# Optimization experiments

Hardware: AMD Instinct MI355X
Metric: run time of the kernel (lower is better)

Reference implementation:

```python
import jax, jax.numpy as jnp
import numpy as np

K = 4
N_UP = 50
N_DOWN = 50


def setup_inputs() -> dict:
    key = jax.random.key(0)
    k1, k2, k3, k4 = jax.random.split(key, 4)
    B, N, D = 2048, 100, 128
    configs = jax.random.randint(k1, (B, N), 0, 4, dtype=jnp.int64)
    tok_table = jax.random.normal(k2, (4, D), dtype=jnp.float32)
    pos_table = jax.random.normal(k3, (144, D), dtype=jnp.float32)
    W_orb = jax.random.normal(k4, (K * (N_UP + N_DOWN), D), dtype=jnp.float32) * 0.01
    b_orb = jnp.zeros((K * (N_UP + N_DOWN),), dtype=jnp.float32)
    return {"configs": configs, "tok_table": tok_table, "pos_table": pos_table,
            "W_orb": W_orb, "b_orb": b_orb}


def _occ_idx(mask, n_occ):
    # indices of occupied sites first (stable argsort of -mask), then sorted ascending
    idx = jnp.argsort(-mask.astype(jnp.float32), axis=1)[:, :n_occ]
    return jnp.sort(idx, axis=1)


def reference(configs, tok_table, pos_table, W_orb, b_orb):
    B, N = configs.shape
    # encode_input + identity backbone
    h = tok_table[configs] + pos_table[jnp.arange(N)][None, :, :]  # (B,N,D)
    orb = jnp.einsum('bnd,od->bno', h, W_orb) + b_orb               # (B,N,K*(nu+nd))
    orb_up = orb[..., :K * N_UP].reshape(B, N, K, N_UP).transpose(0, 2, 1, 3)
    orb_dn = orb[..., K * N_UP:].reshape(B, N, K, N_DOWN).transpose(0, 2, 1, 3)
    has_up = (configs == 1) | (configs == 3)
    has_dn = (configs == 2) | (configs == 3)
    up_idx = _occ_idx(has_up, N_UP)      # (B,n_up)
    dn_idx = _occ_idx(has_dn, N_DOWN)    # (B,n_down)
    phi_up = jnp.take_along_axis(orb_up, up_idx[:, None, :, None], axis=2)  # (B,K,nu,nu)
    phi_dn = jnp.take_along_axis(orb_dn, dn_idx[:, None, :, None], axis=2)  # (B,K,nd,nd)
    det_up = jnp.linalg.det(phi_up)  # (B,K)
    det_dn = jnp.linalg.det(phi_dn)  # (B,K)
    psi = jnp.sum(det_up * det_dn, axis=1)  # (B,)
    log_abs = jnp.log(jnp.abs(psi) + 1e-30)
    phase = jnp.where(psi >= 0, 0.0, jnp.pi).astype(jnp.float32)
    return jax.lax.complex(log_abs.astype(jnp.float32), phase)
```

## Files before the change

kernel.cpp:

```cpp
#include <hip/hip_runtime.h>
#include <math.h>

#define NSITE 100
#define NOCC  50
#define DIM   128
#define KDET  4
#define NTAB  400
#define TP_FLOATS ((4 + 144) * NTAB)


__device__ __forceinline__ unsigned dpp_max64_to_lane63(unsigned x) {
  unsigned t;
  t = (unsigned)__builtin_amdgcn_update_dpp((int)x, (int)x, 0x111, 0xf, 0xf, false);
  x = x > t ? x : t;
  t = (unsigned)__builtin_amdgcn_update_dpp((int)x, (int)x, 0x112, 0xf, 0xf, false);
  x = x > t ? x : t;
  t = (unsigned)__builtin_amdgcn_update_dpp((int)x, (int)x, 0x114, 0xf, 0xf, false);
  x = x > t ? x : t;
  t = (unsigned)__builtin_amdgcn_update_dpp((int)x, (int)x, 0x118, 0xf, 0xf, false);
  x = x > t ? x : t;
  t = (unsigned)__builtin_amdgcn_update_dpp((int)x, (int)x, 0x142, 0xa, 0xf, false);
  x = x > t ? x : t;
  t = (unsigned)__builtin_amdgcn_update_dpp((int)x, (int)x, 0x143, 0xc, 0xf, false);
  x = x > t ? x : t;
  return x;
}

#define REPB(X) X(0) X(1) X(2) X(3) X(4) X(5) X(6) X(7) X(8) X(9) \
  X(10) X(11) X(12) X(13) X(14) X(15) X(16) X(17) X(18) X(19) \
  X(20) X(21) X(22) X(23) X(24) X(25) X(26) X(27) X(28) X(29) \
  X(30) X(31) X(32) X(33) X(34) X(35) X(36) X(37) X(38) X(39) \
  X(40) X(41) X(42) X(43) X(44) X(45) X(46) X(47) X(48) X(49)

#define LUPAIR(X) \
  X(0,1) X(1,2) X(2,3) X(3,4) X(4,5) X(5,6) X(6,7) X(7,8) X(8,9) X(9,10) \
  X(10,11) X(11,12) X(12,13) X(13,14) X(14,15) X(15,16) X(16,17) X(17,18) \
  X(18,19) X(19,20) X(20,21) X(21,22) X(22,23) X(23,24) X(24,25) X(25,26) \
  X(26,27) X(27,28) X(28,29) X(29,30) X(30,31) X(31,32) X(32,33) X(33,34) \
  X(34,35) X(35,36) X(36,37) X(37,38) X(38,39) X(39,40) X(40,41) X(41,42) \
  X(42,43) X(43,44) X(44,45) X(45,46) X(46,47) X(47,48) X(48,49)

__global__ __launch_bounds__(256) void tp_kernel(
    const float* __restrict__ tok, const float* __restrict__ pos,
    const float* __restrict__ W,   const float* __restrict__ bvec,
    float* __restrict__ T, float* __restrict__ P)
{
  const int gid = blockIdx.x * 256 + threadIdx.x;
  if (gid >= 148 * NTAB) return;
  const int row = gid / NTAB;
  const int col = gid - row * NTAB;
  const float4* h4 = (const float4*)((row < 4) ? (tok + (size_t)row * DIM)
                                               : (pos + (size_t)(row - 4) * DIM));
  const float4* w4 = (const float4*)(W + (size_t)col * DIM);
  float acc = 0.0f;
  #pragma unroll
  for (int i = 0; i < DIM / 4; ++i) {
    float4 a = h4[i], b = w4[i];
    acc = fmaf(a.x, b.x, acc);
    acc = fmaf(a.y, b.y, acc);
    acc = fmaf(a.z, b.z, acc);
    acc = fmaf(a.w, b.w, acc);
  }
  if (row < 4) T[(size_t)row * NTAB + col] = acc;
  else         P[(size_t)(row - 4) * NTAB + col] = acc + bvec[col];
}

__global__ __launch_bounds__(256)
__attribute__((amdgpu_waves_per_eu(7)))
void det_kernel(
    const int*   __restrict__ configs,
    const float* __restrict__ T,
    const float* __restrict__ P,
    double*      __restrict__ dets)
{
  const int b    = blockIdx.x;
  const int spin = blockIdx.y;

  __shared__ int cfg[NSITE];
  __shared__ int idx[NOCC];
  __shared__ unsigned long long omask[2];

  const int tid = threadIdx.x;

  bool occv = false;
  if (tid < NSITE) {
    const int c = configs[(size_t)b * NSITE + tid];
    cfg[tid] = c;
    occv = (spin == 0) ? (c == 1 || c == 3) : (c == 2 || c == 3);
  }
  const unsigned long long bal = __ballot(occv);
  if ((tid & 63) == 0 && tid < 128) omask[tid >> 6] = bal;
  __syncthreads();
  if (tid < NSITE) {
    const unsigned long long m0 = omask[0], m1 = omask[1];
    const int mtot = __popcll(m0) + __popcll(m1);
    const int need = (mtot < NOCC) ? (NOCC - mtot) : 0;
    int pocc;
    if (tid >= 64) pocc = __popcll(m0) + __popcll(m1 & ((1ull << (tid - 64)) - 1ull));
    else           pocc = __popcll(m0 & ((1ull << tid) - 1ull));
    const int punocc = tid - pocc;
    const bool sel = occv ? (pocc < NOCC) : (punocc < need);
    const int  poscap = (pocc  < NOCC) ? pocc  : NOCC;
    const int  pfill  = (punocc < need) ? punocc : need;
    if (sel) idx[poscap + pfill] = tid;
  }
  __syncthreads();

  const int lane = tid & 63;
  const int wave = tid >> 6;
  const int wave_u  = __builtin_amdgcn_readfirstlane(wave);
  const int colbase = spin * 200 + wave_u * 50;

  const bool act  = (lane < NOCC);
  const int  site = idx[act ? lane : 0];
  const int  cc0  = cfg[site];
  const float2* T2 = (const float2*)(T + (size_t)cc0  * NTAB + colbase);
  const float2* P2 = (const float2*)(P + (size_t)site * NTAB + colbase);

  #define DECLQ(i) float q##i;
  REPB(DECLQ)
  #undef DECLQ
  #define LQ(i0, i1) { float2 a = T2[(i0) / 2], c = P2[(i0) / 2]; \
      q##i0 = a.x + c.x; q##i1 = a.y + c.y; }
  LQ(0, 1)  LQ(2, 3)  LQ(4, 5)  LQ(6, 7)  LQ(8, 9)  LQ(10, 11)
  __builtin_amdgcn_sched_barrier(0);
  LQ(12, 13) LQ(14, 15) LQ(16, 17) LQ(18, 19) LQ(20, 21) LQ(22, 23)
  __builtin_amdgcn_sched_barrier(0);
  LQ(24, 25) LQ(26, 27) LQ(28, 29) LQ(30, 31) LQ(32, 33) LQ(34, 35)
  __builtin_amdgcn_sched_barrier(0);
  LQ(36, 37) LQ(38, 39) LQ(40, 41) LQ(42, 43) LQ(44, 45) LQ(46, 47)
  __builtin_amdgcn_sched_barrier(0);
  LQ(48, 49)
  #undef LQ

  #define ZEROQ(i) q##i = act ? q##i : 0.0f;
  REPB(ZEROQ)
  #undef ZEROQ

  unsigned aliveq = act ? 0xFFFFFFFFu : 0u;
  float    mant_prod = 1.0f;
  int      esum = 0;
  unsigned sgnx = 0u;
  unsigned long long chosen = 0ull;
  int      invsum = 0;
  const unsigned lu = (unsigned)lane;

  unsigned keyv;
  int   p;
  float rp;

  #define PIVFIN(Jx) { \
    p = __builtin_amdgcn_readlane((int)keyv, 63) & 63; \
    const float piv = __int_as_float( \
        __builtin_amdgcn_readlane(__float_as_int(q##Jx), p)); \
    const unsigned pb = __float_as_uint(piv); \
    esum += (int)((pb >> 23) & 0xFFu) - 127; \
    sgnx ^= (pb & 0x80000000u); \
    mant_prod *= __uint_as_float((pb & 0x007FFFFFu) | 0x3F800000u); \
    invsum += __popcll(chosen >> (p + 1)); \
    chosen |= 1ull << (unsigned)p; \
    aliveq = ((unsigned)lane == (unsigned)p) ? 0u : aliveq; \
    float r0 = __builtin_amdgcn_rcpf(piv); \
    r0 = fmaf(fmaf(-piv, r0, 1.0f), r0, r0); \
    rp = ((pb & 0x7FFFFFFFu) != 0u) ? r0 : 0.0f; }

  #define UPDC(CC) if ((CC) > cJ1) { \
      const float pc = __int_as_float( \
          __builtin_amdgcn_readlane(__float_as_int(q##CC), p)); \
      q##CC = fmaf(-mult, pc, q##CC); }

  #define LUS(J, J1) { \
    const float mult = __uint_as_float(__float_as_uint(q##J * rp) & aliveq); \
    { const float pc0 = __int_as_float( \
          __builtin_amdgcn_readlane(__float_as_int(q##J1), p)); \
      q##J1 = fmaf(-mult, pc0, q##J1); } \
    keyv = ((__float_as_uint(q##J1) & 0x7FFFFFC0u) | lu) & aliveq; \
    keyv = dpp_max64_to_lane63(keyv); \
    const int cJ1 = (J1); \
    REPB(UPDC) \
    PIVFIN(J1) \
  }

  keyv = ((__float_as_uint(q0) & 0x7FFFFFC0u) | lu) & aliveq;
  keyv = dpp_max64_to_lane63(keyv);
  PIVFIN(0)
  LUPAIR(LUS)
  #undef LUS
  #undef UPDC
  #undef PIVFIN

  const double logdet =
      log((double)mant_prod) + (double)esum * 0.6931471805599453;
  const int sgn = (((sgnx >> 31) + (unsigned)invsum) & 1u) ? -1 : 1;

  if (lane == 0) {
    size_t o = (((size_t)b * 2 + spin) * KDET + wave) * 2;
    dets[o]     = logdet;
    dets[o + 1] = (double)sgn;
  }
}

__global__ __launch_bounds__(256) void combine_kernel(
    const double* __restrict__ dets, float* __restrict__ out, int B)
{
  int b = blockIdx.x * blockDim.x + threadIdx.x;
  if (b >= B) return;
  const double* du = dets + ((size_t)b * 2 + 0) * KDET * 2;
  const double* dd = dets + ((size_t)b * 2 + 1) * KDET * 2;
  double t[KDET], s[KDET], m = -1e300;
  #pragma unroll
  for (int k = 0; k < KDET; ++k) {
    t[k] = du[2 * k] + dd[2 * k];
    s[k] = du[2 * k + 1] * dd[2 * k + 1];
    if (t[k] > m) m = t[k];
  }
  double sum = 0.0;
  #pragma unroll
  for (int k = 0; k < KDET; ++k) {
    if (t[k] > -1e290) sum += s[k] * exp(t[k] - m);
  }
  double p  = (m > -1e290) ? exp(m) * fabs(sum) : 0.0;
  double la = log(p + 1e-30);
  float phase = (sum >= 0.0) ? 0.0f : 3.14159265358979f;
  out[b]     = (float)la;
  out[B + b] = phase;
}

extern "C" void kernel_launch(void* const* d_in, const int* in_sizes, int n_in,
                              void* d_out, int out_size, void* d_ws, size_t ws_size,
                              hipStream_t stream) {
  const int*   configs = (const int*)  d_in[0];
  const float* tok     = (const float*)d_in[1];
  const float* pos     = (const float*)d_in[2];
  const float* W       = (const float*)d_in[3];
  const float* bv      = (const float*)d_in[4];

  float*  wsf  = (float*)d_ws;
  float*  T    = wsf;
  float*  P    = wsf + 4 * NTAB;
  double* dets = (double*)(wsf + TP_FLOATS);
  const int B = in_sizes[0] / NSITE;

  tp_kernel<<<(148 * NTAB + 255) / 256, 256, 0, stream>>>(tok, pos, W, bv, T, P);
  dim3 grid(B, 2);
  det_kernel<<<grid, 256, 0, stream>>>(configs, T, P, dets);
  combine_kernel<<<(B + 255) / 256, 256, 0, stream>>>(dets, (float*)d_out, B);
}
```

Before: 230.0 us.

## Split each 50x50 LU across two waves with LDS-broadcast pivot multipliers

Each determinant's 50 columns are now split across two waves by column parity, so each wave holds 25 registers instead of 50. The grid doubles along z so each block handles two determinants. At every elimination step the owning wave picks the pivot and writes multipliers and pivot metadata to shared memory, and both waves then update their columns. The aim is lower register pressure (waves_per_eu raised to 8) and more parallel waves, at the cost of 50 block-wide barriers per LU and LDS traffic on the serial critical path.

```diff
diff --git a/kernel.cpp b/kernel.cpp
--- a/kernel.cpp
+++ b/kernel.cpp
@@ -26,19 +26,9 @@
   return x;
 }
 
-#define REPB(X) X(0) X(1) X(2) X(3) X(4) X(5) X(6) X(7) X(8) X(9) \
+#define REPC(X) X(0) X(1) X(2) X(3) X(4) X(5) X(6) X(7) X(8) X(9) \
   X(10) X(11) X(12) X(13) X(14) X(15) X(16) X(17) X(18) X(19) \
-  X(20) X(21) X(22) X(23) X(24) X(25) X(26) X(27) X(28) X(29) \
-  X(30) X(31) X(32) X(33) X(34) X(35) X(36) X(37) X(38) X(39) \
-  X(40) X(41) X(42) X(43) X(44) X(45) X(46) X(47) X(48) X(49)
-
-#define LUPAIR(X) \
-  X(0,1) X(1,2) X(2,3) X(3,4) X(4,5) X(5,6) X(6,7) X(7,8) X(8,9) X(9,10) \
-  X(10,11) X(11,12) X(12,13) X(13,14) X(14,15) X(15,16) X(16,17) X(17,18) \
-  X(18,19) X(19,20) X(20,21) X(21,22) X(22,23) X(23,24) X(24,25) X(25,26) \
-  X(26,27) X(27,28) X(28,29) X(29,30) X(30,31) X(31,32) X(32,33) X(33,34) \
-  X(34,35) X(35,36) X(36,37) X(37,38) X(38,39) X(39,40) X(40,41) X(41,42) \
-  X(42,43) X(43,44) X(44,45) X(45,46) X(46,47) X(47,48) X(48,49)
+  X(20) X(21) X(22) X(23) X(24)
 
 __global__ __launch_bounds__(256) void tp_kernel(
     const float* __restrict__ tok, const float* __restrict__ pos,
@@ -66,7 +56,7 @@
 }
 
 __global__ __launch_bounds__(256)
-__attribute__((amdgpu_waves_per_eu(7)))
+__attribute__((amdgpu_waves_per_eu(8)))
 void det_kernel(
     const int*   __restrict__ configs,
     const float* __restrict__ T,
@@ -79,6 +69,8 @@
   __shared__ int cfg[NSITE];
   __shared__ int idx[NOCC];
   __shared__ unsigned long long omask[2];
+  __shared__ float mbuf[2][2][64];
+  __shared__ int   meta[2][2][2];
 
   const int tid = threadIdx.x;
 
@@ -106,35 +98,28 @@
   }
   __syncthreads();
 
-  const int lane = tid & 63;
-  const int wave = tid >> 6;
-  const int wave_u  = __builtin_amdgcn_readfirstlane(wave);
-  const int colbase = spin * 200 + wave_u * 50;
+  const int lane  = tid & 63;
+  const int wave  = tid >> 6;
+  const int dloc  = __builtin_amdgcn_readfirstlane(wave >> 1);
+  const int h     = __builtin_amdgcn_readfirstlane(wave & 1);
+  const int k     = blockIdx.z * 2 + dloc;
+  const int colbase = spin * 200 + k * 50;
 
   const bool act  = (lane < NOCC);
   const int  site = idx[act ? lane : 0];
   const int  cc0  = cfg[site];
-  const float2* T2 = (const float2*)(T + (size_t)cc0  * NTAB + colbase);
-  const float2* P2 = (const float2*)(P + (size_t)site * NTAB + colbase);
+  const float* Trow = T + (size_t)cc0  * NTAB + colbase + h;
+  const float* Prow = P + (size_t)site * NTAB + colbase + h;
 
   #define DECLQ(i) float q##i;
-  REPB(DECLQ)
+  REPC(DECLQ)
   #undef DECLQ
-  #define LQ(i0, i1) { float2 a = T2[(i0) / 2], c = P2[(i0) / 2]; \
-      q##i0 = a.x + c.x; q##i1 = a.y + c.y; }
-  LQ(0, 1)  LQ(2, 3)  LQ(4, 5)  LQ(6, 7)  LQ(8, 9)  LQ(10, 11)
-  __builtin_amdgcn_sched_barrier(0);
-  LQ(12, 13) LQ(14, 15) LQ(16, 17) LQ(18, 19) LQ(20, 21) LQ(22, 23)
-  __builtin_amdgcn_sched_barrier(0);
-  LQ(24, 25) LQ(26, 27) LQ(28, 29) LQ(30, 31) LQ(32, 33) LQ(34, 35)
-  __builtin_amdgcn_sched_barrier(0);
-  LQ(36, 37) LQ(38, 39) LQ(40, 41) LQ(42, 43) LQ(44, 45) LQ(46, 47)
-  __builtin_amdgcn_sched_barrier(0);
-  LQ(48, 49)
+  #define LQ(i) q##i = Trow[2 * (i)] + Prow[2 * (i)];
+  REPC(LQ)
   #undef LQ
 
   #define ZEROQ(i) q##i = act ? q##i : 0.0f;
-  REPB(ZEROQ)
+  REPC(ZEROQ)
   #undef ZEROQ
 
   unsigned aliveq = act ? 0xFFFFFFFFu : 0u;
@@ -145,56 +130,86 @@
   int      invsum = 0;
   const unsigned lu = (unsigned)lane;
 
-  unsigned keyv;
-  int   p;
-  float rp;
-
-  #define PIVFIN(Jx) { \
-    p = __builtin_amdgcn_readlane((int)keyv, 63) & 63; \
-    const float piv = __int_as_float( \
-        __builtin_amdgcn_readlane(__float_as_int(q##Jx), p)); \
-    const unsigned pb = __float_as_uint(piv); \
-    esum += (int)((pb >> 23) & 0xFFu) - 127; \
-    sgnx ^= (pb & 0x80000000u); \
-    mant_prod *= __uint_as_float((pb & 0x007FFFFFu) | 0x3F800000u); \
-    invsum += __popcll(chosen >> (p + 1)); \
-    chosen |= 1ull << (unsigned)p; \
-    aliveq = ((unsigned)lane == (unsigned)p) ? 0u : aliveq; \
-    float r0 = __builtin_amdgcn_rcpf(piv); \
-    r0 = fmaf(fmaf(-piv, r0, 1.0f), r0, r0); \
-    rp = ((pb & 0x7FFFFFFFu) != 0u) ? r0 : 0.0f; }
-
-  #define UPDC(CC) if ((CC) > cJ1) { \
-      const float pc = __int_as_float( \
-          __builtin_amdgcn_readlane(__float_as_int(q##CC), p)); \
-      q##CC = fmaf(-mult, pc, q##CC); }
-
-  #define LUS(J, J1) { \
-    const float mult = __uint_as_float(__float_as_uint(q##J * rp) & aliveq); \
-    { const float pc0 = __int_as_float( \
-          __builtin_amdgcn_readlane(__float_as_int(q##J1), p)); \
-      q##J1 = fmaf(-mult, pc0, q##J1); } \
-    keyv = ((__float_as_uint(q##J1) & 0x7FFFFFC0u) | lu) & aliveq; \
-    keyv = dpp_max64_to_lane63(keyv); \
-    const int cJ1 = (J1); \
-    REPB(UPDC) \
-    PIVFIN(J1) \
-  }
-
-  keyv = ((__float_as_uint(q0) & 0x7FFFFFC0u) | lu) & aliveq;
-  keyv = dpp_max64_to_lane63(keyv);
-  PIVFIN(0)
-  LUPAIR(LUS)
-  #undef LUS
-  #undef UPDC
-  #undef PIVFIN
+  #define UPD(L) { const float pc = __int_as_float( \
+      __builtin_amdgcn_readlane(__float_as_int(q##L), p)); \
+      q##L = fmaf(-mult, pc, q##L); }
+
+  #define UPDFROM_24 UPD(24)
+  #define UPDFROM_23 UPD(23) UPDFROM_24
+  #define UPDFROM_22 UPD(22) UPDFROM_23
+  #define UPDFROM_21 UPD(21) UPDFROM_22
+  #define UPDFROM_20 UPD(20) UPDFROM_21
+  #define UPDFROM_19 UPD(19) UPDFROM_20
+  #define UPDFROM_18 UPD(18) UPDFROM_19
+  #define UPDFROM_17 UPD(17) UPDFROM_18
+  #define UPDFROM_16 UPD(16) UPDFROM_17
+  #define UPDFROM_15 UPD(15) UPDFROM_16
+  #define UPDFROM_14 UPD(14) UPDFROM_15
+  #define UPDFROM_13 UPD(13) UPDFROM_14
+  #define UPDFROM_12 UPD(12) UPDFROM_13
+  #define UPDFROM_11 UPD(11) UPDFROM_12
+  #define UPDFROM_10 UPD(10) UPDFROM_11
+  #define UPDFROM_9  UPD(9)  UPDFROM_10
+  #define UPDFROM_8  UPD(8)  UPDFROM_9
+  #define UPDFROM_7  UPD(7)  UPDFROM_8
+  #define UPDFROM_6  UPD(6)  UPDFROM_7
+  #define UPDFROM_5  UPD(5)  UPDFROM_6
+  #define UPDFROM_4  UPD(4)  UPDFROM_5
+  #define UPDFROM_3  UPD(3)  UPDFROM_4
+  #define UPDFROM_2  UPD(2)  UPDFROM_3
+  #define UPDFROM_1  UPD(1)  UPDFROM_2
+  #define UPDFROM_0  UPD(0)  UPDFROM_1
+
+  #define STEP(L0, PAR) { \
+    if (h == (PAR)) { \
+      unsigned key = ((__float_as_uint(q##L0) & 0x7FFFFFC0u) | lu) & aliveq; \
+      key = dpp_max64_to_lane63(key); \
+      const int pp = __builtin_amdgcn_readlane((int)key, 63) & 63; \
+      const unsigned pvb = (unsigned)__builtin_amdgcn_readlane( \
+          __float_as_int(q##L0), pp); \
+      const float piv = __uint_as_float(pvb); \
+      float r0 = __builtin_amdgcn_rcpf(piv); \
+      r0 = fmaf(fmaf(-piv, r0, 1.0f), r0, r0); \
+      const float rp = ((pvb & 0x7FFFFFFFu) != 0u) ? r0 : 0.0f; \
+      const unsigned am = aliveq & ((lane == pp) ? 0u : 0xFFFFFFFFu); \
+      const float mv = __uint_as_float(__float_as_uint(q##L0 * rp) & am); \
+      mbuf[PAR][dloc][lane] = mv; \
+      if (lane == 0) { meta[PAR][dloc][0] = pp; meta[PAR][dloc][1] = (int)pvb; } \
+    } \
+    __syncthreads(); \
+    { \
+      const float mult = mbuf[PAR][dloc][lane]; \
+      const int   pv0  = meta[PAR][dloc][0]; \
+      const int   pv1  = meta[PAR][dloc][1]; \
+      const int      p  = __builtin_amdgcn_readfirstlane(pv0); \
+      const unsigned pb = (unsigned)__builtin_amdgcn_readfirstlane(pv1); \
+      esum += (int)((pb >> 23) & 0xFFu) - 127; \
+      sgnx ^= (pb & 0x80000000u); \
+      mant_prod *= __uint_as_float((pb & 0x007FFFFFu) | 0x3F800000u); \
+      invsum += __popcll(chosen >> (p + 1)); \
+      chosen |= 1ull << (unsigned)p; \
+      aliveq = (lane == p) ? 0u : aliveq; \
+      UPDFROM_##L0 \
+    } }
+
+  STEP(0,0)   STEP(0,1)   STEP(1,0)   STEP(1,1)   STEP(2,0)   STEP(2,1)
+  STEP(3,0)   STEP(3,1)   STEP(4,0)   STEP(4,1)   STEP(5,0)   STEP(5,1)
+  STEP(6,0)   STEP(6,1)   STEP(7,0)   STEP(7,1)   STEP(8,0)   STEP(8,1)
+  STEP(9,0)   STEP(9,1)   STEP(10,0)  STEP(10,1)  STEP(11,0)  STEP(11,1)
+  STEP(12,0)  STEP(12,1)  STEP(13,0)  STEP(13,1)  STEP(14,0)  STEP(14,1)
+  STEP(15,0)  STEP(15,1)  STEP(16,0)  STEP(16,1)  STEP(17,0)  STEP(17,1)
+  STEP(18,0)  STEP(18,1)  STEP(19,0)  STEP(19,1)  STEP(20,0)  STEP(20,1)
+  STEP(21,0)  STEP(21,1)  STEP(22,0)  STEP(22,1)  STEP(23,0)  STEP(23,1)
+  STEP(24,0)  STEP(24,1)
+  #undef STEP
+  #undef UPD
 
   const double logdet =
       log((double)mant_prod) + (double)esum * 0.6931471805599453;
   const int sgn = (((sgnx >> 31) + (unsigned)invsum) & 1u) ? -1 : 1;
 
-  if (lane == 0) {
-    size_t o = (((size_t)b * 2 + spin) * KDET + wave) * 2;
+  if (h == 0 && lane == 0) {
+    size_t o = (((size_t)b * 2 + spin) * KDET + k) * 2;
     dets[o]     = logdet;
     dets[o + 1] = (double)sgn;
   }
@@ -242,7 +257,7 @@
   const int B = in_sizes[0] / NSITE;
 
   tp_kernel<<<(148 * NTAB + 255) / 256, 256, 0, stream>>>(tok, pos, W, bv, T, P);
-  dim3 grid(B, 2);
+  dim3 grid(B, 2, 2);
   det_kernel<<<grid, 256, 0, stream>>>(configs, T, P, dets);
   combine_kernel<<<(B + 255) / 256, 256, 0, stream>>>(dets, (float*)d_out, B);
 }
```

New measurement: 255.0 us. +10.8%, slower.
